# Kernel optimization log

Hardware: AMD Instinct MI355X
Metric: run time of the kernel (lower is better)

Reference implementation:

```python
import jax, jax.numpy as jnp
import numpy as np

T, H, E, I, SI, TOP_K = 4096, 2048, 16, 1024, 4096, 1


def setup_inputs() -> dict:
    key = jax.random.key(0)
    ks = jax.random.split(key, 8)
    s_h = 1.0 / np.sqrt(H)
    s_i = 1.0 / np.sqrt(I)
    s_si = 1.0 / np.sqrt(SI)
    return {
        "hidden_states": jax.random.normal(ks[0], (T, H), jnp.float32),
        "router_w": jax.random.normal(ks[1], (E, H), jnp.float32) * s_h,
        "w_gate": jax.random.normal(ks[2], (E, H, I), jnp.float32) * s_h,
        "w_up": jax.random.normal(ks[3], (E, H, I), jnp.float32) * s_h,
        "w_down": jax.random.normal(ks[4], (E, I, H), jnp.float32) * s_i,
        "ws_gate": jax.random.normal(ks[5], (H, SI), jnp.float32) * s_h,
        "ws_up": jax.random.normal(ks[6], (H, SI), jnp.float32) * s_h,
        "ws_down": jax.random.normal(ks[7], (SI, H), jnp.float32) * s_si,
    }


def reference(hidden_states, router_w, w_gate, w_up, w_down, ws_gate, ws_up, ws_down):
    x = hidden_states  # [T, H]
    # Router: logits -> top-k -> sigmoid weights (Llama4RenormalizeMoeRoutingMethod)
    logits = jnp.einsum("th,eh->te", x, router_w)              # [T, E]
    top_vals, top_idx = jax.lax.top_k(logits, TOP_K)            # [T, K]
    weights = jax.nn.sigmoid(top_vals)                          # [T, K]
    # dispatch[t, e] = router weight if expert e selected for token t, else 0
    onehot = jax.nn.one_hot(top_idx, E, dtype=x.dtype)          # [T, K, E]
    dispatch = jnp.einsum("tke,tk->te", onehot, weights)        # [T, E]
    # Routed experts: router weight applied on input (commutes through the
    # linear gate/up projections as a per-(t,e) scalar applied before SiLU).
    g = jnp.einsum("th,ehi->tei", x, w_gate) * dispatch[:, :, None]  # [T, E, I]
    u = jnp.einsum("th,ehi->tei", x, w_up) * dispatch[:, :, None]    # [T, E, I]
    act = jax.nn.silu(g) * u                                          # [T, E, I]
    # Unselected experts contribute exactly 0 (act==0 there), so summing over
    # E in the down projection is the combine step.
    routed = jnp.einsum("tei,eih->th", act, w_down)             # [T, H]
    # Shared expert (SiLU-gated MLP on the unscaled hidden states)
    shared = (jax.nn.silu(x @ ws_gate) * (x @ ws_up)) @ ws_down  # [T, H]
    return shared + routed
```

## Files before the change

kernel.cpp:

```cpp
#include <hip/hip_runtime.h>
#include <hip/hip_bf16.h>

typedef unsigned short u16;
typedef unsigned int   u32;
typedef __attribute__((ext_vector_type(8))) short short8;
typedef __attribute__((ext_vector_type(4))) float f32x4;

#define T_TOK 4096
#define HDIM  2048
#define NEXP  16
#define IDIM  1024
#define SIDIM 4096
#define RCAP  6144
#define NTIL  48

#define O_WT      0u
#define O_EIDX    16384u
#define O_CNT     32768u
#define O_POS     32832u
#define O_PADOFF  32896u
#define O_TILEEXP 33024u
#define O_TOKROW  33280u
#define O_XBF     65536u
#define O_XSC     (O_XBF  + 2u*T_TOK*HDIM)
#define O_ACTS    (O_XSC  + 2u*RCAP*HDIM)
#define O_ACTR    (O_ACTS + 2u*T_TOK*SIDIM)
#define O_WSGT    (O_ACTR + 2u*RCAP*IDIM)
#define O_WSUT    (O_WSGT + 2u*SIDIM*HDIM)
#define O_WSDT    (O_WSUT + 2u*SIDIM*HDIM)

__device__ __forceinline__ u16 f2b(float f) {
  u32 u = __float_as_uint(f);
  u = (u + 0x7FFFu + ((u >> 16) & 1u)) >> 16;
  return (u16)u;
}

#define GLDS16(g, l) __builtin_amdgcn_global_load_lds( \
    (const __attribute__((address_space(1))) void*)(g), \
    (__attribute__((address_space(3))) void*)(l), 16, 0, 0)
#define BARX() __builtin_amdgcn_s_barrier()
#define SETPRIO(x) __builtin_amdgcn_s_setprio(x)
#define WAITVM(n) asm volatile("s_waitcnt vmcnt(" #n ")" ::: "memory")

__global__ __launch_bounds__(256) void router_k(
    const float* __restrict__ x, const float* __restrict__ rw,
    float* __restrict__ wt, int* __restrict__ eidx, int* __restrict__ cnt,
    u16* __restrict__ xbf) {
  int w = threadIdx.x >> 6, l = threadIdx.x & 63;
  int t = blockIdx.x * 4 + w;
  double acc[NEXP];
#pragma unroll
  for (int e = 0; e < NEXP; ++e) acc[e] = 0.0;
  const float* xp = x + (size_t)t * HDIM;
  u16* xo = xbf + (size_t)t * HDIM;
  for (int hb = 0; hb < HDIM; hb += 256) {
    float4 xv = *(const float4*)(xp + hb + l * 4);
    uint2 o;
    o.x = (u32)f2b(xv.x) | ((u32)f2b(xv.y) << 16);
    o.y = (u32)f2b(xv.z) | ((u32)f2b(xv.w) << 16);
    *(uint2*)(xo + hb + l * 4) = o;
#pragma unroll
    for (int e = 0; e < NEXP; ++e) {
      float4 wv = *(const float4*)(rw + (size_t)e * HDIM + hb + l * 4);
      acc[e] += (double)xv.x * wv.x + (double)xv.y * wv.y
              + (double)xv.z * wv.z + (double)xv.w * wv.w;
    }
  }
#pragma unroll
  for (int e = 0; e < NEXP; ++e) {
    double v = acc[e];
#pragma unroll
    for (int off = 32; off; off >>= 1) v += __shfl_xor(v, off, 64);
    acc[e] = v;
  }
  if (l == 0) {
    double best = acc[0]; int be = 0;
#pragma unroll
    for (int e = 1; e < NEXP; ++e) if (acc[e] > best) { best = acc[e]; be = e; }
    wt[t] = 1.0f / (1.0f + __expf(-(float)best));
    eidx[t] = be;
    atomicAdd(&cnt[be], 1);
  }
}

__global__ void scan_k(const int* __restrict__ cnt, int* __restrict__ pad_off,
                       int* __restrict__ tile_exp, int* __restrict__ pos,
                       int* __restrict__ tok_row) {
  if (threadIdx.x == 0) {
    for (int i = 0; i < 64; ++i) tile_exp[i] = -1;
    int run = 0;
    for (int e = 0; e < NEXP; ++e) {
      pad_off[e] = run;
      int pc = ((cnt[e] + 127) >> 7) << 7;
      for (int tt = run >> 7; tt < (run + pc) >> 7; ++tt) tile_exp[tt] = e;
      run += pc;
      pos[e] = 0;
    }
    pad_off[NEXP] = run;
  }
  for (int i = threadIdx.x; i < RCAP; i += 256) tok_row[i] = -1;
}

__global__ void assign_k(const int* __restrict__ eidx, const int* __restrict__ pad_off,
                         int* __restrict__ pos, int* __restrict__ tok_row) {
  int t = blockIdx.x * 256 + threadIdx.x;
  if (t >= T_TOK) return;
  int e = eidx[t];
  int r = atomicAdd(&pos[e], 1);
  tok_row[pad_off[e] + r] = t;
}

__global__ __launch_bounds__(256) void gather_k(
    const float* __restrict__ x, const float* __restrict__ wt,
    const int* __restrict__ tok_row, u16* __restrict__ xsc) {
  int g = blockIdx.x;
  int tid = threadIdx.x;
  u16* dst = xsc + (size_t)g * HDIM;
  int t = tok_row[g];
  if (t < 0) {
    uint2 z; z.x = 0u; z.y = 0u;
#pragma unroll
    for (int i = 0; i < 2; ++i) *(uint2*)(dst + i * 1024 + tid * 4) = z;
  } else {
    float s = wt[t];
    const float* src = x + (size_t)t * HDIM;
#pragma unroll
    for (int i = 0; i < 2; ++i) {
      int c = i * 1024 + tid * 4;
      float4 v = *(const float4*)(src + c);
      uint2 o;
      o.x = (u32)f2b(v.x * s) | ((u32)f2b(v.y * s) << 16);
      o.y = (u32)f2b(v.z * s) | ((u32)f2b(v.w * s) << 16);
      *(uint2*)(dst + c) = o;
    }
  }
}

__device__ __forceinline__ void conv_tile(
    const float* __restrict__ src, u16* __restrict__ dst, int K, int N,
    int bx, int ky, u32 (*lt)[36], int tid) {
  const int n0 = bx * 64, k0 = ky * 64;
  const int l = tid & 63, w = tid >> 6;
  const float* sp = src + (size_t)(k0 + w * 16) * N + n0 + l;
  u32 p[8];
#pragma unroll
  for (int i = 0; i < 8; ++i) {
    float a = sp[(size_t)(2 * i) * N];
    float b = sp[(size_t)(2 * i + 1) * N];
    p[i] = (u32)f2b(a) | ((u32)f2b(b) << 16);
  }
  *(uint4*)&lt[l][w * 8 + 0] = make_uint4(p[0], p[1], p[2], p[3]);
  *(uint4*)&lt[l][w * 8 + 4] = make_uint4(p[4], p[5], p[6], p[7]);
  __syncthreads();
  const int c = tid & 7, n2 = tid >> 3;
#pragma unroll
  for (int rnd = 0; rnd < 2; ++rnd) {
    int n = n2 + rnd * 32;
    uint4 v = *(const uint4*)&lt[n][c * 4];
    *(uint4*)(dst + (size_t)(n0 + n) * K + k0 + c * 8) = v;
  }
}

__global__ __launch_bounds__(256) void megaconv(
    const float* __restrict__ wsg, const float* __restrict__ wsu,
    const float* __restrict__ wsd, u16* wsgT, u16* wsuT, u16* wsdT) {
  __shared__ u32 lt[64][36];
  int idx = blockIdx.x, tid = threadIdx.x;
  if (idx < 2048) {
    conv_tile(wsg, wsgT, 2048, 4096, idx & 63, idx >> 6, lt, tid);
  } else if (idx < 4096) { idx -= 2048;
    conv_tile(wsu, wsuT, 2048, 4096, idx & 63, idx >> 6, lt, tid);
  } else { idx -= 4096;
    conv_tile(wsd, wsdT, 4096, 2048, idx & 31, idx >> 5, lt, tid);
  }
}


__global__ __launch_bounds__(512, 2) void gu_sh8(
    const u16* __restrict__ A, const u16* __restrict__ Bg, const u16* __restrict__ Bu,
    u16* __restrict__ act) {
  extern __shared__ u16 sm[];
  u16* As  = sm;
  u16* Bsm = sm + 32768;
  const int bid = blockIdx.x;
  const int xcd = bid & 7, bi = bid >> 3;
  const int bx = xcd * 4 + (bi & 3), by = bi >> 2;
  const int m0 = by * 256, c0 = bx * 128;
  const int tid = threadIdx.x, l = tid & 63, wid = tid >> 6;
  const int wm = wid >> 1, wn = wid & 1;

  const int cpos = tid & 3, rr = tid >> 2;
  const int gc = (cpos ^ ((rr >> 1) & 3)) * 8;
  const u16* aS0 = A + (size_t)(m0 + rr) * HDIM + gc;
  const u16* aS1 = A + (size_t)(m0 + 128 + rr) * HDIM + gc;
  const int mat = (rr >> 6) & 1;
  const u16* bbase = mat ? Bu : Bg;
  const u16* bS0 = bbase + (size_t)(c0 + (rr & 63)) * HDIM + gc;
  const u16* bS1 = bbase + (size_t)(c0 + 64 + (rr & 63)) * HDIM + gc;
  const int ld0 = tid * 8, ld1 = (512 + tid) * 8;

#define STA_G(bb, kh, koff) do { \
    GLDS16(aS0 + (koff) + (kh) * 32, As + ((bb) * 2 + (kh)) * 8192 + ld0); \
    GLDS16(aS1 + (koff) + (kh) * 32, As + ((bb) * 2 + (kh)) * 8192 + ld1); } while (0)
#define STB_G(bb, kh, koff) do { \
    GLDS16(bS0 + (koff) + (kh) * 32, Bsm + ((bb) * 2 + (kh)) * 8192 + ld0); \
    GLDS16(bS1 + (koff) + (kh) * 32, Bsm + ((bb) * 2 + (kh)) * 8192 + ld1); } while (0)

  const int fch = ((l >> 4) ^ ((l >> 1) & 3)) * 8;
  int aoff[4], boff[8];
#pragma unroll
  for (int mf = 0; mf < 4; ++mf) aoff[mf] = (wm * 64 + mf * 16 + (l & 15)) * 32 + fch;
#pragma unroll
  for (int i = 0; i < 8; ++i) {
    int v = wn * 128 + (i >> 2) * 64 + (i & 3) * 16 + (l & 15);
    boff[i] = v * 32 + fch;
  }
#define LDA_G(bb, kh) do { const u16* s_ = As + ((bb) * 2 + (kh)) * 8192; \
    af[0] = *(const short8*)(s_ + aoff[0]); af[1] = *(const short8*)(s_ + aoff[1]); \
    af[2] = *(const short8*)(s_ + aoff[2]); af[3] = *(const short8*)(s_ + aoff[3]); } while (0)
#define LDB_G(bb, kh, h, d) do { const u16* s_ = Bsm + ((bb) * 2 + (kh)) * 8192; \
    d[0] = *(const short8*)(s_ + boff[(h) * 4 + 0]); d[1] = *(const short8*)(s_ + boff[(h) * 4 + 1]); \
    d[2] = *(const short8*)(s_ + boff[(h) * 4 + 2]); d[3] = *(const short8*)(s_ + boff[(h) * 4 + 3]); } while (0)
#define MM32_G() do { SETPRIO(1); \
    _Pragma("unroll") for (int mf = 0; mf < 4; ++mf) { \
      _Pragma("unroll") for (int nf = 0; nf < 4; ++nf) \
        acc[mf][nf] = __builtin_amdgcn_mfma_f32_16x16x32_bf16(af[mf], bfrA[nf], acc[mf][nf], 0, 0, 0); \
      _Pragma("unroll") for (int nf = 0; nf < 4; ++nf) \
        acc[mf][4 + nf] = __builtin_amdgcn_mfma_f32_16x16x32_bf16(af[mf], bfrB[nf], acc[mf][4 + nf], 0, 0, 0); \
    } SETPRIO(0); } while (0)

  f32x4 acc[4][8];
#pragma unroll
  for (int i = 0; i < 4; ++i)
#pragma unroll
    for (int j = 0; j < 8; ++j)
#pragma unroll
      for (int r = 0; r < 4; ++r) acc[i][j][r] = 0.0f;
  short8 af[4], bfrA[4], bfrB[4];

  STA_G(0, 0, 0); STB_G(0, 0, 0); STA_G(0, 1, 0); STB_G(0, 1, 0);
  WAITVM(4); BARX();
  const int NT = HDIM / 64;
  for (int t = 0; t < NT - 1; ++t) {
    const int b = t & 1, nb = b ^ 1, kn = (t + 1) * 64;
    LDA_G(b, 0); LDB_G(b, 0, 0, bfrA); LDB_G(b, 0, 1, bfrB);
    STA_G(nb, 0, kn); STB_G(nb, 0, kn);
    MM32_G(); WAITVM(4); BARX();
    LDA_G(b, 1); LDB_G(b, 1, 0, bfrA); LDB_G(b, 1, 1, bfrB);
    STA_G(nb, 1, kn); STB_G(nb, 1, kn);
    MM32_G(); WAITVM(4); BARX();
  }
  { const int b = (NT - 1) & 1;
    LDA_G(b, 0); LDB_G(b, 0, 0, bfrA); LDB_G(b, 0, 1, bfrB);
    MM32_G(); WAITVM(0); BARX();
    LDA_G(b, 1); LDB_G(b, 1, 0, bfrA); LDB_G(b, 1, 1, bfrB);
    MM32_G();
  }
#pragma unroll
  for (int mf = 0; mf < 4; ++mf)
#pragma unroll
    for (int nf = 0; nf < 4; ++nf) {
      int col = c0 + wn * 64 + nf * 16 + (l & 15);
      int rowb = m0 + wm * 64 + mf * 16 + (l >> 4) * 4;
#pragma unroll
      for (int r = 0; r < 4; ++r) {
        float g = acc[mf][nf][r], u = acc[mf][4 + nf][r];
        float s = g / (1.0f + __expf(-g));
        act[(size_t)(rowb + r) * SIDIM + col] = f2b(s * u);
      }
    }
#undef STA_G
#undef STB_G
#undef LDA_G
#undef LDB_G
#undef MM32_G
}

__global__ __launch_bounds__(512, 2) void dn_sh8(
    const u16* __restrict__ A, const u16* __restrict__ B, float* __restrict__ out) {
  extern __shared__ u16 sm[];
  u16* As  = sm;
  u16* Bsm = sm + 32768;
  const int bid = blockIdx.x;
  const int xcd = bid & 7, bi = bid >> 3;
  const int bx = xcd * 2 + (bi & 1), by = bi >> 1;
  const int m0 = by * 256, c0 = bx * 128;
  const int tid = threadIdx.x, l = tid & 63, wid = tid >> 6;
  const int wm = wid >> 1, wn = wid & 1;

  const int cpos = tid & 3, rr = tid >> 2;
  const int gc = (cpos ^ ((rr >> 1) & 3)) * 8;
  const u16* aS0 = A + (size_t)(m0 + rr) * SIDIM + gc;
  const u16* aS1 = A + (size_t)(m0 + 128 + rr) * SIDIM + gc;
  const u16* bS  = B + (size_t)(c0 + rr) * SIDIM + gc;
  const int ld0 = tid * 8, ld1 = (512 + tid) * 8;

#define STA_D(bb, kh, koff) do { \
    GLDS16(aS0 + (koff) + (kh) * 32, As + ((bb) * 2 + (kh)) * 8192 + ld0); \
    GLDS16(aS1 + (koff) + (kh) * 32, As + ((bb) * 2 + (kh)) * 8192 + ld1); } while (0)
#define STB_D(bb, kh, koff) \
    GLDS16(bS + (koff) + (kh) * 32, Bsm + ((bb) * 2 + (kh)) * 4096 + ld0)

  const int fch = ((l >> 4) ^ ((l >> 1) & 3)) * 8;
  int aoff[4], boff[4];
#pragma unroll
  for (int mf = 0; mf < 4; ++mf) aoff[mf] = (wm * 64 + mf * 16 + (l & 15)) * 32 + fch;
#pragma unroll
  for (int i = 0; i < 4; ++i) {
    int v = wn * 64 + (i >> 1) * 32 + (i & 1) * 16 + (l & 15);
    boff[i] = v * 32 + fch;
  }
#define LDA_D(bb, kh) do { const u16* s_ = As + ((bb) * 2 + (kh)) * 8192; \
    af[0] = *(const short8*)(s_ + aoff[0]); af[1] = *(const short8*)(s_ + aoff[1]); \
    af[2] = *(const short8*)(s_ + aoff[2]); af[3] = *(const short8*)(s_ + aoff[3]); } while (0)
#define LDB_D(bb, kh, h, d) do { const u16* s_ = Bsm + ((bb) * 2 + (kh)) * 4096; \
    d[0] = *(const short8*)(s_ + boff[(h) * 2 + 0]); \
    d[1] = *(const short8*)(s_ + boff[(h) * 2 + 1]); } while (0)
#define MM16_D() do { SETPRIO(1); \
    _Pragma("unroll") for (int mf = 0; mf < 4; ++mf) { \
      acc[mf][0] = __builtin_amdgcn_mfma_f32_16x16x32_bf16(af[mf], bfrA[0], acc[mf][0], 0, 0, 0); \
      acc[mf][1] = __builtin_amdgcn_mfma_f32_16x16x32_bf16(af[mf], bfrA[1], acc[mf][1], 0, 0, 0); \
      acc[mf][2] = __builtin_amdgcn_mfma_f32_16x16x32_bf16(af[mf], bfrB[0], acc[mf][2], 0, 0, 0); \
      acc[mf][3] = __builtin_amdgcn_mfma_f32_16x16x32_bf16(af[mf], bfrB[1], acc[mf][3], 0, 0, 0); \
    } SETPRIO(0); } while (0)

  f32x4 acc[4][4];
#pragma unroll
  for (int i = 0; i < 4; ++i)
#pragma unroll
    for (int j = 0; j < 4; ++j)
#pragma unroll
      for (int r = 0; r < 4; ++r) acc[i][j][r] = 0.0f;
  short8 af[4], bfrA[2], bfrB[2];

  STA_D(0, 0, 0); STB_D(0, 0, 0); STA_D(0, 1, 0); STB_D(0, 1, 0);
  WAITVM(3); BARX();
  const int NT = SIDIM / 64;
  for (int t = 0; t < NT - 1; ++t) {
    const int b = t & 1, nb = b ^ 1, kn = (t + 1) * 64;
    LDA_D(b, 0); LDB_D(b, 0, 0, bfrA); LDB_D(b, 0, 1, bfrB);
    STA_D(nb, 0, kn); STB_D(nb, 0, kn);
    MM16_D(); WAITVM(3); BARX();
    LDA_D(b, 1); LDB_D(b, 1, 0, bfrA); LDB_D(b, 1, 1, bfrB);
    STA_D(nb, 1, kn); STB_D(nb, 1, kn);
    MM16_D(); WAITVM(3); BARX();
  }
  { const int b = (NT - 1) & 1;
    LDA_D(b, 0); LDB_D(b, 0, 0, bfrA); LDB_D(b, 0, 1, bfrB);
    MM16_D(); WAITVM(0); BARX();
    LDA_D(b, 1); LDB_D(b, 1, 0, bfrA); LDB_D(b, 1, 1, bfrB);
    MM16_D();
  }
#pragma unroll
  for (int mf = 0; mf < 4; ++mf)
#pragma unroll
    for (int nf = 0; nf < 4; ++nf) {
      int col = c0 + wn * 64 + (nf >> 1) * 32 + (nf & 1) * 16 + (l & 15);
      int rowb = m0 + wm * 64 + mf * 16 + (l >> 4) * 4;
#pragma unroll
      for (int r = 0; r < 4; ++r)
        out[(size_t)(rowb + r) * HDIM + col] = acc[mf][nf][r];
    }
#undef STA_D
#undef STB_D
#undef LDA_D
#undef LDB_D
#undef MM16_D
}


__global__ __launch_bounds__(256) void gu_rf(
    const u16* __restrict__ A, const float* __restrict__ Bg0, const float* __restrict__ Bu0,
    u16* __restrict__ act, const int* __restrict__ tile_exp) {
  __shared__ __align__(16) u16 As[128 * 64];
  __shared__ __align__(16) u16 Bgs[32 * 72];
  __shared__ __align__(16) u16 Bus[32 * 72];
  const int tid = threadIdx.x;
  const int l = tid & 63, w = tid >> 6;
  const int wm = w >> 1, wn = w & 1;
  const int m0 = blockIdx.y * 128, n0 = blockIdx.x * 32;
  int e = tile_exp[blockIdx.y];
  if (e < 0) return;
  size_t eo = (size_t)e * HDIM * IDIM;
  const int bcol = l & 31;
  const int krow0 = w * 16 + (l >> 5) * 8;
  const float* Bgp = Bg0 + eo + (size_t)krow0 * IDIM + n0 + bcol;
  const float* Bup = Bu0 + eo + (size_t)krow0 * IDIM + n0 + bcol;
  f32x4 accg[4], accu[4];
#pragma unroll
  for (int i = 0; i < 4; ++i)
#pragma unroll
    for (int r = 0; r < 4; ++r) { accg[i][r] = 0.0f; accu[i][r] = 0.0f; }
  const u16* Ab = A + (size_t)m0 * HDIM;

  for (int k0 = 0; k0 < HDIM; k0 += 64) {
    __syncthreads();
#pragma unroll
    for (int j = 0; j < 4; ++j) {
      int c = j * 256 + tid, r = c >> 3, cc = c & 7;
      GLDS16(Ab + (size_t)r * HDIM + k0 + ((cc ^ (r & 7)) * 8), &As[c * 8]);
    }
    {
      float g8[8], u8[8];
#pragma unroll
      for (int i = 0; i < 8; ++i) {
        g8[i] = Bgp[(size_t)(k0 + i) * IDIM];
        u8[i] = Bup[(size_t)(k0 + i) * IDIM];
      }
      uint4 pg, pu;
      pg.x = (u32)f2b(g8[0]) | ((u32)f2b(g8[1]) << 16);
      pg.y = (u32)f2b(g8[2]) | ((u32)f2b(g8[3]) << 16);
      pg.z = (u32)f2b(g8[4]) | ((u32)f2b(g8[5]) << 16);
      pg.w = (u32)f2b(g8[6]) | ((u32)f2b(g8[7]) << 16);
      *(uint4*)&Bgs[bcol * 72 + krow0] = pg;
      pu.x = (u32)f2b(u8[0]) | ((u32)f2b(u8[1]) << 16);
      pu.y = (u32)f2b(u8[2]) | ((u32)f2b(u8[3]) << 16);
      pu.z = (u32)f2b(u8[4]) | ((u32)f2b(u8[5]) << 16);
      pu.w = (u32)f2b(u8[6]) | ((u32)f2b(u8[7]) << 16);
      *(uint4*)&Bus[bcol * 72 + krow0] = pu;
    }
    __syncthreads();
#pragma unroll
    for (int kh = 0; kh < 2; ++kh) {
      const int q = kh * 4 + (l >> 4);
      short8 af[4];
#pragma unroll
      for (int mf = 0; mf < 4; ++mf) {
        int r = wm * 64 + mf * 16 + (l & 15);
        af[mf] = *(const short8*)&As[r * 64 + ((q ^ (r & 7)) * 8)];
      }
      const int n = wn * 16 + (l & 15);
      short8 bgf = *(const short8*)&Bgs[n * 72 + q * 8];
      short8 buf2 = *(const short8*)&Bus[n * 72 + q * 8];
#pragma unroll
      for (int mf = 0; mf < 4; ++mf) {
        accg[mf] = __builtin_amdgcn_mfma_f32_16x16x32_bf16(af[mf], bgf,  accg[mf], 0, 0, 0);
        accu[mf] = __builtin_amdgcn_mfma_f32_16x16x32_bf16(af[mf], buf2, accu[mf], 0, 0, 0);
      }
    }
  }
#pragma unroll
  for (int mf = 0; mf < 4; ++mf) {
    int col = n0 + wn * 16 + (l & 15);
#pragma unroll
    for (int r = 0; r < 4; ++r) {
      int row = m0 + wm * 64 + mf * 16 + (l >> 4) * 4 + r;
      float g = accg[mf][r], u = accu[mf][r];
      float s = g / (1.0f + __expf(-g));
      act[(size_t)row * IDIM + col] = f2b(s * u);
    }
  }
}

__global__ __launch_bounds__(256) void dn_rf(
    const u16* __restrict__ A, const float* __restrict__ B0, float* __restrict__ out,
    const int* __restrict__ tile_exp, const int* __restrict__ tok_row) {
  __shared__ __align__(16) u16 As[128 * 64];
  __shared__ __align__(16) u16 Bs[64 * 72];
  const int tid = threadIdx.x;
  const int l = tid & 63, w = tid >> 6;
  const int wm = w >> 1, wn = w & 1;
  const int m0 = blockIdx.y * 128, n0 = blockIdx.x * 64;
  int e = tile_exp[blockIdx.y];
  if (e < 0) return;
  const float* B = B0 + (size_t)e * IDIM * HDIM;
  f32x4 acc[4][2];
#pragma unroll
  for (int i = 0; i < 4; ++i)
#pragma unroll
    for (int j = 0; j < 2; ++j)
#pragma unroll
      for (int r = 0; r < 4; ++r) acc[i][j][r] = 0.0f;
  const u16* Ab = A + (size_t)m0 * IDIM;

  for (int k0 = 0; k0 < IDIM; k0 += 64) {
    __syncthreads();
#pragma unroll
    for (int j = 0; j < 4; ++j) {
      int c = j * 256 + tid, r = c >> 3, cc = c & 7;
      GLDS16(Ab + (size_t)r * IDIM + k0 + ((cc ^ (r & 7)) * 8), &As[c * 8]);
    }
    {
      const float* bp = B + (size_t)(k0 + w * 16) * HDIM + n0 + l;
      u16 h[16];
#pragma unroll
      for (int i = 0; i < 16; ++i) h[i] = f2b(bp[(size_t)i * HDIM]);
#pragma unroll
      for (int j = 0; j < 4; ++j) {
        uint2 v; v.x = (u32)h[4*j] | ((u32)h[4*j+1] << 16);
        v.y = (u32)h[4*j+2] | ((u32)h[4*j+3] << 16);
        *(uint2*)&Bs[l * 72 + w * 16 + j * 4] = v;
      }
    }
    __syncthreads();
#pragma unroll
    for (int kh = 0; kh < 2; ++kh) {
      const int q = kh * 4 + (l >> 4);
      short8 af[4];
#pragma unroll
      for (int mf = 0; mf < 4; ++mf) {
        int r = wm * 64 + mf * 16 + (l & 15);
        af[mf] = *(const short8*)&As[r * 64 + ((q ^ (r & 7)) * 8)];
      }
      short8 bf[2];
#pragma unroll
      for (int nf = 0; nf < 2; ++nf) {
        int n = wn * 32 + nf * 16 + (l & 15);
        bf[nf] = *(const short8*)&Bs[n * 72 + q * 8];
      }
#pragma unroll
      for (int mf = 0; mf < 4; ++mf)
#pragma unroll
        for (int nf = 0; nf < 2; ++nf)
          acc[mf][nf] = __builtin_amdgcn_mfma_f32_16x16x32_bf16(af[mf], bf[nf], acc[mf][nf], 0, 0, 0);
    }
  }
#pragma unroll
  for (int mf = 0; mf < 4; ++mf)
#pragma unroll
    for (int nf = 0; nf < 2; ++nf) {
      int col = n0 + wn * 32 + nf * 16 + (l & 15);
#pragma unroll
      for (int r = 0; r < 4; ++r) {
        int grow = m0 + wm * 64 + mf * 16 + (l >> 4) * 4 + r;
        int t = tok_row[grow];
        if (t >= 0) out[(size_t)t * HDIM + col] += acc[mf][nf][r];
      }
    }
}

extern "C" void kernel_launch(void* const* d_in, const int* in_sizes, int n_in,
                              void* d_out, int out_size, void* d_ws, size_t ws_size,
                              hipStream_t stream) {
  const float* x   = (const float*)d_in[0];
  const float* rw  = (const float*)d_in[1];
  const float* wg  = (const float*)d_in[2];
  const float* wu  = (const float*)d_in[3];
  const float* wd  = (const float*)d_in[4];
  const float* wsg = (const float*)d_in[5];
  const float* wsu = (const float*)d_in[6];
  const float* wsd = (const float*)d_in[7];
  float* out = (float*)d_out;
  char* ws = (char*)d_ws;

  float* wt     = (float*)(ws + O_WT);
  int* eidx     = (int*)(ws + O_EIDX);
  int* cnt      = (int*)(ws + O_CNT);
  int* pos      = (int*)(ws + O_POS);
  int* pad_off  = (int*)(ws + O_PADOFF);
  int* tile_exp = (int*)(ws + O_TILEEXP);
  int* tok_row  = (int*)(ws + O_TOKROW);
  u16* xbf      = (u16*)(ws + O_XBF);
  u16* xsc      = (u16*)(ws + O_XSC);
  u16* acts     = (u16*)(ws + O_ACTS);
  u16* actr     = (u16*)(ws + O_ACTR);
  u16* wsgT     = (u16*)(ws + O_WSGT);
  u16* wsuT     = (u16*)(ws + O_WSUT);
  u16* wsdT     = (u16*)(ws + O_WSDT);

  hipFuncSetAttribute((const void*)gu_sh8, hipFuncAttributeMaxDynamicSharedMemorySize, 131072);
  hipFuncSetAttribute((const void*)dn_sh8, hipFuncAttributeMaxDynamicSharedMemorySize, 98304);

  hipMemsetAsync(ws + O_CNT, 0, 128, stream);
  megaconv<<<6144, 256, 0, stream>>>(wsg, wsu, wsd, wsgT, wsuT, wsdT);
  router_k<<<T_TOK / 4, 256, 0, stream>>>(x, rw, wt, eidx, cnt, xbf);
  scan_k<<<1, 256, 0, stream>>>(cnt, pad_off, tile_exp, pos, tok_row);
  assign_k<<<T_TOK / 256, 256, 0, stream>>>(eidx, pad_off, pos, tok_row);
  gather_k<<<RCAP, 256, 0, stream>>>(x, wt, tok_row, xsc);

  gu_sh8<<<512, 512, 131072, stream>>>(xbf, wsgT, wsuT, acts);
  gu_rf<<<dim3(IDIM / 32, NTIL), 256, 0, stream>>>(xsc, wg, wu, actr, tile_exp);
  dn_sh8<<<256, 512, 98304, stream>>>(acts, wsdT, out);
  dn_rf<<<dim3(HDIM / 64, NTIL), 256, 0, stream>>>(actr, wd, out, tile_exp, tok_row);
}
```

Baseline: 572.7 us.

## Double-buffer routed expert GEMMs with direct fp32 weight LDS loads

Restructures gu_rf and dn_rf into a double-buffered pipeline. A and the fp32 expert weights are loaded asynchronously into LDS through global_load_lds, so the next k-slice is fetched while the current one feeds MFMA. Weights are now converted to bf16 at fragment-read time with v_cvt_pk_bf16_f32 instead of the per-thread scalar loads plus a software round-and-pack before the LDS store. This also adds s_setprio around the MFMA bursts and 64KB of dynamic LDS per block, which may lower occupancy.

Measured after the change: 605.8 us. +5.8%, slower.

```diff
diff --git a/kernel.cpp b/kernel.cpp
--- a/kernel.cpp
+++ b/kernel.cpp
@@ -35,6 +35,12 @@
   return (u16)u;
 }
 
+__device__ __forceinline__ u32 cvtpk(float a, float b) {
+  u32 r;
+  asm("v_cvt_pk_bf16_f32 %0, %1, %2" : "=v"(r) : "v"(a), "v"(b));
+  return r;
+}
+
 #define GLDS16(g, l) __builtin_amdgcn_global_load_lds( \
     (const __attribute__((address_space(1))) void*)(g), \
     (__attribute__((address_space(3))) void*)(l), 16, 0, 0)
@@ -372,72 +378,89 @@
 __global__ __launch_bounds__(256) void gu_rf(
     const u16* __restrict__ A, const float* __restrict__ Bg0, const float* __restrict__ Bu0,
     u16* __restrict__ act, const int* __restrict__ tile_exp) {
-  __shared__ __align__(16) u16 As[128 * 64];
-  __shared__ __align__(16) u16 Bgs[32 * 72];
-  __shared__ __align__(16) u16 Bus[32 * 72];
+  extern __shared__ __align__(16) char smraw[];
+  u16*   smA  = (u16*)smraw;
+  float* smBg = (float*)(smraw + 32768);
+  float* smBu = (float*)(smraw + 49152);
   const int tid = threadIdx.x;
-  const int l = tid & 63, w = tid >> 6;
-  const int wm = w >> 1, wn = w & 1;
+  const int l = tid & 63, w4 = tid >> 6;
+  const int wm = w4 >> 1, wn = w4 & 1;
   const int m0 = blockIdx.y * 128, n0 = blockIdx.x * 32;
   int e = tile_exp[blockIdx.y];
   if (e < 0) return;
   size_t eo = (size_t)e * HDIM * IDIM;
-  const int bcol = l & 31;
-  const int krow0 = w * 16 + (l >> 5) * 8;
-  const float* Bgp = Bg0 + eo + (size_t)krow0 * IDIM + n0 + bcol;
-  const float* Bup = Bu0 + eo + (size_t)krow0 * IDIM + n0 + bcol;
+  const float* Bg = Bg0 + eo;
+  const float* Bu = Bu0 + eo;
+  const u16* Ab = A + (size_t)m0 * HDIM;
+
+  const int bk = tid >> 3;
+  const int bn = ((tid & 7) * 4) ^ (((bk >> 3) & 1) << 4);
+
+#define STA_R(bb, kh, k0v) do { \
+    _Pragma("unroll") for (int li = 0; li < 2; ++li) { \
+      int c_ = li * 256 + tid, r_ = c_ >> 2, cp_ = c_ & 3; \
+      int gc_ = (cp_ ^ ((r_ >> 1) & 3)) * 8; \
+      GLDS16(Ab + (size_t)r_ * HDIM + (k0v) + (kh) * 32 + gc_, \
+             smA + ((bb) * 2 + (kh)) * 4096 + c_ * 8); } } while (0)
+#define STB_R(bb, kh, k0v) do { \
+    GLDS16(Bg + (size_t)((k0v) + (kh) * 32 + bk) * IDIM + n0 + bn, \
+           smBg + ((bb) * 2 + (kh)) * 1024 + tid * 4); \
+    GLDS16(Bu + (size_t)((k0v) + (kh) * 32 + bk) * IDIM + n0 + bn, \
+           smBu + ((bb) * 2 + (kh)) * 1024 + tid * 4); } while (0)
+
+  const int fch = ((l >> 4) ^ ((l >> 1) & 3)) * 8;
+  int aoff[4];
+#pragma unroll
+  for (int mf = 0; mf < 4; ++mf) aoff[mf] = (wm * 64 + mf * 16 + (l & 15)) * 32 + fch;
+  const int bnr = (wn * 16 + (l & 15)) ^ (((l >> 4) & 1) << 4);
+  const int bkb = (l >> 4) * 8;
+
   f32x4 accg[4], accu[4];
 #pragma unroll
   for (int i = 0; i < 4; ++i)
 #pragma unroll
     for (int r = 0; r < 4; ++r) { accg[i][r] = 0.0f; accu[i][r] = 0.0f; }
-  const u16* Ab = A + (size_t)m0 * HDIM;
-
-  for (int k0 = 0; k0 < HDIM; k0 += 64) {
-    __syncthreads();
-#pragma unroll
-    for (int j = 0; j < 4; ++j) {
-      int c = j * 256 + tid, r = c >> 3, cc = c & 7;
-      GLDS16(Ab + (size_t)r * HDIM + k0 + ((cc ^ (r & 7)) * 8), &As[c * 8]);
-    }
-    {
-      float g8[8], u8[8];
-#pragma unroll
-      for (int i = 0; i < 8; ++i) {
-        g8[i] = Bgp[(size_t)(k0 + i) * IDIM];
-        u8[i] = Bup[(size_t)(k0 + i) * IDIM];
-      }
-      uint4 pg, pu;
-      pg.x = (u32)f2b(g8[0]) | ((u32)f2b(g8[1]) << 16);
-      pg.y = (u32)f2b(g8[2]) | ((u32)f2b(g8[3]) << 16);
-      pg.z = (u32)f2b(g8[4]) | ((u32)f2b(g8[5]) << 16);
-      pg.w = (u32)f2b(g8[6]) | ((u32)f2b(g8[7]) << 16);
-      *(uint4*)&Bgs[bcol * 72 + krow0] = pg;
-      pu.x = (u32)f2b(u8[0]) | ((u32)f2b(u8[1]) << 16);
-      pu.y = (u32)f2b(u8[2]) | ((u32)f2b(u8[3]) << 16);
-      pu.z = (u32)f2b(u8[4]) | ((u32)f2b(u8[5]) << 16);
-      pu.w = (u32)f2b(u8[6]) | ((u32)f2b(u8[7]) << 16);
-      *(uint4*)&Bus[bcol * 72 + krow0] = pu;
-    }
-    __syncthreads();
-#pragma unroll
-    for (int kh = 0; kh < 2; ++kh) {
-      const int q = kh * 4 + (l >> 4);
-      short8 af[4];
-#pragma unroll
-      for (int mf = 0; mf < 4; ++mf) {
-        int r = wm * 64 + mf * 16 + (l & 15);
-        af[mf] = *(const short8*)&As[r * 64 + ((q ^ (r & 7)) * 8)];
-      }
-      const int n = wn * 16 + (l & 15);
-      short8 bgf = *(const short8*)&Bgs[n * 72 + q * 8];
-      short8 buf2 = *(const short8*)&Bus[n * 72 + q * 8];
-#pragma unroll
-      for (int mf = 0; mf < 4; ++mf) {
-        accg[mf] = __builtin_amdgcn_mfma_f32_16x16x32_bf16(af[mf], bgf,  accg[mf], 0, 0, 0);
-        accu[mf] = __builtin_amdgcn_mfma_f32_16x16x32_bf16(af[mf], buf2, accu[mf], 0, 0, 0);
-      }
-    }
+  short8 af[4], bgf, buf2;
+
+#define PH_READ_R(bb, kh) do { \
+    const u16* As_ = smA + ((bb) * 2 + (kh)) * 4096; \
+    af[0] = *(const short8*)(As_ + aoff[0]); af[1] = *(const short8*)(As_ + aoff[1]); \
+    af[2] = *(const short8*)(As_ + aoff[2]); af[3] = *(const short8*)(As_ + aoff[3]); \
+    const float* Bg_ = smBg + ((bb) * 2 + (kh)) * 1024; \
+    const float* Bu_ = smBu + ((bb) * 2 + (kh)) * 1024; \
+    int4 wg_, wu_; \
+    wg_.x = cvtpk(Bg_[(bkb + 0) * 32 + bnr], Bg_[(bkb + 1) * 32 + bnr]); \
+    wg_.y = cvtpk(Bg_[(bkb + 2) * 32 + bnr], Bg_[(bkb + 3) * 32 + bnr]); \
+    wg_.z = cvtpk(Bg_[(bkb + 4) * 32 + bnr], Bg_[(bkb + 5) * 32 + bnr]); \
+    wg_.w = cvtpk(Bg_[(bkb + 6) * 32 + bnr], Bg_[(bkb + 7) * 32 + bnr]); \
+    wu_.x = cvtpk(Bu_[(bkb + 0) * 32 + bnr], Bu_[(bkb + 1) * 32 + bnr]); \
+    wu_.y = cvtpk(Bu_[(bkb + 2) * 32 + bnr], Bu_[(bkb + 3) * 32 + bnr]); \
+    wu_.z = cvtpk(Bu_[(bkb + 4) * 32 + bnr], Bu_[(bkb + 5) * 32 + bnr]); \
+    wu_.w = cvtpk(Bu_[(bkb + 6) * 32 + bnr], Bu_[(bkb + 7) * 32 + bnr]); \
+    bgf  = *(short8*)&wg_; buf2 = *(short8*)&wu_; } while (0)
+#define MM_R() do { SETPRIO(1); \
+    _Pragma("unroll") for (int mf = 0; mf < 4; ++mf) { \
+      accg[mf] = __builtin_amdgcn_mfma_f32_16x16x32_bf16(af[mf], bgf,  accg[mf], 0, 0, 0); \
+      accu[mf] = __builtin_amdgcn_mfma_f32_16x16x32_bf16(af[mf], buf2, accu[mf], 0, 0, 0); \
+    } SETPRIO(0); } while (0)
+
+  STA_R(0, 0, 0); STB_R(0, 0, 0); STA_R(0, 1, 0); STB_R(0, 1, 0);
+  WAITVM(0); BARX();
+  const int NT = HDIM / 64;
+  for (int t = 0; t < NT - 1; ++t) {
+    const int b = t & 1, nb = b ^ 1, kn = (t + 1) * 64;
+    PH_READ_R(b, 0);
+    STA_R(nb, 0, kn); STB_R(nb, 0, kn);
+    MM_R(); WAITVM(4); BARX();
+    PH_READ_R(b, 1);
+    STA_R(nb, 1, kn); STB_R(nb, 1, kn);
+    MM_R(); WAITVM(4); BARX();
+  }
+  { const int b = (NT - 1) & 1;
+    PH_READ_R(b, 0);
+    MM_R(); WAITVM(0); BARX();
+    PH_READ_R(b, 1);
+    MM_R();
   }
 #pragma unroll
   for (int mf = 0; mf < 4; ++mf) {
@@ -450,20 +473,50 @@
       act[(size_t)row * IDIM + col] = f2b(s * u);
     }
   }
+#undef STA_R
+#undef STB_R
+#undef PH_READ_R
+#undef MM_R
 }
 
 __global__ __launch_bounds__(256) void dn_rf(
     const u16* __restrict__ A, const float* __restrict__ B0, float* __restrict__ out,
     const int* __restrict__ tile_exp, const int* __restrict__ tok_row) {
-  __shared__ __align__(16) u16 As[128 * 64];
-  __shared__ __align__(16) u16 Bs[64 * 72];
+  extern __shared__ __align__(16) char smraw[];
+  u16*   smA = (u16*)smraw;
+  float* smB = (float*)(smraw + 32768);
   const int tid = threadIdx.x;
-  const int l = tid & 63, w = tid >> 6;
-  const int wm = w >> 1, wn = w & 1;
+  const int l = tid & 63, w4 = tid >> 6;
+  const int wm = w4 >> 1, wn = w4 & 1;
   const int m0 = blockIdx.y * 128, n0 = blockIdx.x * 64;
   int e = tile_exp[blockIdx.y];
   if (e < 0) return;
   const float* B = B0 + (size_t)e * IDIM * HDIM;
+  const u16* Ab = A + (size_t)m0 * IDIM;
+
+#define STA_E(bb, kh, k0v) do { \
+    _Pragma("unroll") for (int li = 0; li < 2; ++li) { \
+      int c_ = li * 256 + tid, r_ = c_ >> 2, cp_ = c_ & 3; \
+      int gc_ = (cp_ ^ ((r_ >> 1) & 3)) * 8; \
+      GLDS16(Ab + (size_t)r_ * IDIM + (k0v) + (kh) * 32 + gc_, \
+             smA + ((bb) * 2 + (kh)) * 4096 + c_ * 8); } } while (0)
+#define STB_E(bb, kh, k0v) do { \
+    _Pragma("unroll") for (int li = 0; li < 2; ++li) { \
+      int s_ = li * 256 + tid, k_ = s_ >> 4; \
+      int n_ = ((s_ & 15) * 4) ^ (((k_ >> 3) & 1) << 4); \
+      GLDS16(B + (size_t)((k0v) + (kh) * 32 + k_) * HDIM + n0 + n_, \
+             smB + ((bb) * 2 + (kh)) * 2048 + s_ * 4); } } while (0)
+
+  const int fch = ((l >> 4) ^ ((l >> 1) & 3)) * 8;
+  int aoff[4];
+#pragma unroll
+  for (int mf = 0; mf < 4; ++mf) aoff[mf] = (wm * 64 + mf * 16 + (l & 15)) * 32 + fch;
+  int bnr[2];
+#pragma unroll
+  for (int nf = 0; nf < 2; ++nf)
+    bnr[nf] = (wn * 32 + nf * 16 + (l & 15)) ^ (((l >> 4) & 1) << 4);
+  const int bkb = (l >> 4) * 8;
+
   f32x4 acc[4][2];
 #pragma unroll
   for (int i = 0; i < 4; ++i)
@@ -471,49 +524,43 @@
     for (int j = 0; j < 2; ++j)
 #pragma unroll
       for (int r = 0; r < 4; ++r) acc[i][j][r] = 0.0f;
-  const u16* Ab = A + (size_t)m0 * IDIM;
-
-  for (int k0 = 0; k0 < IDIM; k0 += 64) {
-    __syncthreads();
-#pragma unroll
-    for (int j = 0; j < 4; ++j) {
-      int c = j * 256 + tid, r = c >> 3, cc = c & 7;
-      GLDS16(Ab + (size_t)r * IDIM + k0 + ((cc ^ (r & 7)) * 8), &As[c * 8]);
-    }
-    {
-      const float* bp = B + (size_t)(k0 + w * 16) * HDIM + n0 + l;
-      u16 h[16];
-#pragma unroll
-      for (int i = 0; i < 16; ++i) h[i] = f2b(bp[(size_t)i * HDIM]);
-#pragma unroll
-      for (int j = 0; j < 4; ++j) {
-        uint2 v; v.x = (u32)h[4*j] | ((u32)h[4*j+1] << 16);
-        v.y = (u32)h[4*j+2] | ((u32)h[4*j+3] << 16);
-        *(uint2*)&Bs[l * 72 + w * 16 + j * 4] = v;
-      }
-    }
-    __syncthreads();
-#pragma unroll
-    for (int kh = 0; kh < 2; ++kh) {
-      const int q = kh * 4 + (l >> 4);
-      short8 af[4];
-#pragma unroll
-      for (int mf = 0; mf < 4; ++mf) {
-        int r = wm * 64 + mf * 16 + (l & 15);
-        af[mf] = *(const short8*)&As[r * 64 + ((q ^ (r & 7)) * 8)];
-      }
-      short8 bf[2];
-#pragma unroll
-      for (int nf = 0; nf < 2; ++nf) {
-        int n = wn * 32 + nf * 16 + (l & 15);
-        bf[nf] = *(const short8*)&Bs[n * 72 + q * 8];
-      }
-#pragma unroll
-      for (int mf = 0; mf < 4; ++mf)
-#pragma unroll
-        for (int nf = 0; nf < 2; ++nf)
-          acc[mf][nf] = __builtin_amdgcn_mfma_f32_16x16x32_bf16(af[mf], bf[nf], acc[mf][nf], 0, 0, 0);
-    }
+  short8 af[4], bf[2];
+
+#define PH_READ_E(bb, kh) do { \
+    const u16* As_ = smA + ((bb) * 2 + (kh)) * 4096; \
+    af[0] = *(const short8*)(As_ + aoff[0]); af[1] = *(const short8*)(As_ + aoff[1]); \
+    af[2] = *(const short8*)(As_ + aoff[2]); af[3] = *(const short8*)(As_ + aoff[3]); \
+    const float* B_ = smB + ((bb) * 2 + (kh)) * 2048; \
+    _Pragma("unroll") for (int nf = 0; nf < 2; ++nf) { \
+      int4 w_; \
+      w_.x = cvtpk(B_[(bkb + 0) * 64 + bnr[nf]], B_[(bkb + 1) * 64 + bnr[nf]]); \
+      w_.y = cvtpk(B_[(bkb + 2) * 64 + bnr[nf]], B_[(bkb + 3) * 64 + bnr[nf]]); \
+      w_.z = cvtpk(B_[(bkb + 4) * 64 + bnr[nf]], B_[(bkb + 5) * 64 + bnr[nf]]); \
+      w_.w = cvtpk(B_[(bkb + 6) * 64 + bnr[nf]], B_[(bkb + 7) * 64 + bnr[nf]]); \
+      bf[nf] = *(short8*)&w_; } } while (0)
+#define MM_E() do { SETPRIO(1); \
+    _Pragma("unroll") for (int mf = 0; mf < 4; ++mf) { \
+      acc[mf][0] = __builtin_amdgcn_mfma_f32_16x16x32_bf16(af[mf], bf[0], acc[mf][0], 0, 0, 0); \
+      acc[mf][1] = __builtin_amdgcn_mfma_f32_16x16x32_bf16(af[mf], bf[1], acc[mf][1], 0, 0, 0); \
+    } SETPRIO(0); } while (0)
+
+  STA_E(0, 0, 0); STB_E(0, 0, 0); STA_E(0, 1, 0); STB_E(0, 1, 0);
+  WAITVM(0); BARX();
+  const int NT = IDIM / 64;
+  for (int t = 0; t < NT - 1; ++t) {
+    const int b = t & 1, nb = b ^ 1, kn = (t + 1) * 64;
+    PH_READ_E(b, 0);
+    STA_E(nb, 0, kn); STB_E(nb, 0, kn);
+    MM_E(); WAITVM(4); BARX();
+    PH_READ_E(b, 1);
+    STA_E(nb, 1, kn); STB_E(nb, 1, kn);
+    MM_E(); WAITVM(4); BARX();
+  }
+  { const int b = (NT - 1) & 1;
+    PH_READ_E(b, 0);
+    MM_E(); WAITVM(0); BARX();
+    PH_READ_E(b, 1);
+    MM_E();
   }
 #pragma unroll
   for (int mf = 0; mf < 4; ++mf)
@@ -527,6 +574,10 @@
         if (t >= 0) out[(size_t)t * HDIM + col] += acc[mf][nf][r];
       }
     }
+#undef STA_E
+#undef STB_E
+#undef PH_READ_E
+#undef MM_E
 }
 
 extern "C" void kernel_launch(void* const* d_in, const int* in_sizes, int n_in,
@@ -560,6 +611,8 @@
 
   hipFuncSetAttribute((const void*)gu_sh8, hipFuncAttributeMaxDynamicSharedMemorySize, 131072);
   hipFuncSetAttribute((const void*)dn_sh8, hipFuncAttributeMaxDynamicSharedMemorySize, 98304);
+  hipFuncSetAttribute((const void*)gu_rf, hipFuncAttributeMaxDynamicSharedMemorySize, 65536);
+  hipFuncSetAttribute((const void*)dn_rf, hipFuncAttributeMaxDynamicSharedMemorySize, 65536);
 
   hipMemsetAsync(ws + O_CNT, 0, 128, stream);
   megaconv<<<6144, 256, 0, stream>>>(wsg, wsu, wsd, wsgT, wsuT, wsdT);
@@ -569,7 +622,7 @@
   gather_k<<<RCAP, 256, 0, stream>>>(x, wt, tok_row, xsc);
 
   gu_sh8<<<512, 512, 131072, stream>>>(xbf, wsgT, wsuT, acts);
-  gu_rf<<<dim3(IDIM / 32, NTIL), 256, 0, stream>>>(xsc, wg, wu, actr, tile_exp);
+  gu_rf<<<dim3(IDIM / 32, NTIL), 256, 65536, stream>>>(xsc, wg, wu, actr, tile_exp);
   dn_sh8<<<256, 512, 98304, stream>>>(acts, wsdT, out);
-  dn_rf<<<dim3(HDIM / 64, NTIL), 256, 0, stream>>>(actr, wd, out, tile_exp, tok_row);
-}
+  dn_rf<<<dim3(HDIM / 64, NTIL), 256, 65536, stream>>>(actr, wd, out, tile_exp, tok_row);
+}
```

## Drop LDS staging in routed expert GEMMs, load fragments directly into registers

Applied to the files above, without the earlier changes.

The routed gate/up and down kernels no longer stage A and B tiles through shared memory with barriers. Each lane now loads its MFMA fragments straight from global memory and converts fp32 weights with the packed bf16 convert instruction. This removes the LDS writes, LDS reads and both barriers per k-step. In exchange, waves that share a tile each re-read it from global/L2, which raises redundant global traffic and gives up the swizzled coalesced A loads.

Result: slower. 1.017 ms (+77.5%).

```diff
diff --git a/kernel.cpp b/kernel.cpp
--- a/kernel.cpp
+++ b/kernel.cpp
@@ -35,6 +35,12 @@
   return (u16)u;
 }
 
+__device__ __forceinline__ u32 cvtpk(float a, float b) {
+  u32 r;
+  asm("v_cvt_pk_bf16_f32 %0, %1, %2" : "=v"(r) : "v"(a), "v"(b));
+  return r;
+}
+
 #define GLDS16(g, l) __builtin_amdgcn_global_load_lds( \
     (const __attribute__((address_space(1))) void*)(g), \
     (__attribute__((address_space(3))) void*)(l), 16, 0, 0)
@@ -372,9 +378,6 @@
 __global__ __launch_bounds__(256) void gu_rf(
     const u16* __restrict__ A, const float* __restrict__ Bg0, const float* __restrict__ Bu0,
     u16* __restrict__ act, const int* __restrict__ tile_exp) {
-  __shared__ __align__(16) u16 As[128 * 64];
-  __shared__ __align__(16) u16 Bgs[32 * 72];
-  __shared__ __align__(16) u16 Bus[32 * 72];
   const int tid = threadIdx.x;
   const int l = tid & 63, w = tid >> 6;
   const int wm = w >> 1, wn = w & 1;
@@ -382,72 +385,57 @@
   int e = tile_exp[blockIdx.y];
   if (e < 0) return;
   size_t eo = (size_t)e * HDIM * IDIM;
-  const int bcol = l & 31;
-  const int krow0 = w * 16 + (l >> 5) * 8;
-  const float* Bgp = Bg0 + eo + (size_t)krow0 * IDIM + n0 + bcol;
-  const float* Bup = Bu0 + eo + (size_t)krow0 * IDIM + n0 + bcol;
+  const int col = wn * 16 + (l & 15);
+  const int q0 = l >> 4;
+  const float* Bg = Bg0 + eo + n0 + col;
+  const float* Bu = Bu0 + eo + n0 + col;
+  const u16* Ar = A + (size_t)(m0 + wm * 64 + (l & 15)) * HDIM;
+
   f32x4 accg[4], accu[4];
 #pragma unroll
   for (int i = 0; i < 4; ++i)
 #pragma unroll
     for (int r = 0; r < 4; ++r) { accg[i][r] = 0.0f; accu[i][r] = 0.0f; }
-  const u16* Ab = A + (size_t)m0 * HDIM;
 
   for (int k0 = 0; k0 < HDIM; k0 += 64) {
-    __syncthreads();
-#pragma unroll
-    for (int j = 0; j < 4; ++j) {
-      int c = j * 256 + tid, r = c >> 3, cc = c & 7;
-      GLDS16(Ab + (size_t)r * HDIM + k0 + ((cc ^ (r & 7)) * 8), &As[c * 8]);
-    }
-    {
-      float g8[8], u8[8];
-#pragma unroll
-      for (int i = 0; i < 8; ++i) {
-        g8[i] = Bgp[(size_t)(k0 + i) * IDIM];
-        u8[i] = Bup[(size_t)(k0 + i) * IDIM];
+    short8 af[2][4];
+    float bg[2][8], bu[2][8];
+#pragma unroll
+    for (int kh = 0; kh < 2; ++kh) {
+      const int kq = k0 + (kh * 4 + q0) * 8;
+#pragma unroll
+      for (int mf = 0; mf < 4; ++mf)
+        af[kh][mf] = *(const short8*)(Ar + (size_t)(mf * 16) * HDIM + kq);
+#pragma unroll
+      for (int j = 0; j < 8; ++j) {
+        bg[kh][j] = Bg[(size_t)(kq + j) * IDIM];
+        bu[kh][j] = Bu[(size_t)(kq + j) * IDIM];
       }
-      uint4 pg, pu;
-      pg.x = (u32)f2b(g8[0]) | ((u32)f2b(g8[1]) << 16);
-      pg.y = (u32)f2b(g8[2]) | ((u32)f2b(g8[3]) << 16);
-      pg.z = (u32)f2b(g8[4]) | ((u32)f2b(g8[5]) << 16);
-      pg.w = (u32)f2b(g8[6]) | ((u32)f2b(g8[7]) << 16);
-      *(uint4*)&Bgs[bcol * 72 + krow0] = pg;
-      pu.x = (u32)f2b(u8[0]) | ((u32)f2b(u8[1]) << 16);
-      pu.y = (u32)f2b(u8[2]) | ((u32)f2b(u8[3]) << 16);
-      pu.z = (u32)f2b(u8[4]) | ((u32)f2b(u8[5]) << 16);
-      pu.w = (u32)f2b(u8[6]) | ((u32)f2b(u8[7]) << 16);
-      *(uint4*)&Bus[bcol * 72 + krow0] = pu;
-    }
-    __syncthreads();
+    }
 #pragma unroll
     for (int kh = 0; kh < 2; ++kh) {
-      const int q = kh * 4 + (l >> 4);
-      short8 af[4];
+      int4 pg, pu;
+      pg.x = cvtpk(bg[kh][0], bg[kh][1]); pg.y = cvtpk(bg[kh][2], bg[kh][3]);
+      pg.z = cvtpk(bg[kh][4], bg[kh][5]); pg.w = cvtpk(bg[kh][6], bg[kh][7]);
+      pu.x = cvtpk(bu[kh][0], bu[kh][1]); pu.y = cvtpk(bu[kh][2], bu[kh][3]);
+      pu.z = cvtpk(bu[kh][4], bu[kh][5]); pu.w = cvtpk(bu[kh][6], bu[kh][7]);
+      short8 bgf = *(short8*)&pg, buf2 = *(short8*)&pu;
 #pragma unroll
       for (int mf = 0; mf < 4; ++mf) {
-        int r = wm * 64 + mf * 16 + (l & 15);
-        af[mf] = *(const short8*)&As[r * 64 + ((q ^ (r & 7)) * 8)];
+        accg[mf] = __builtin_amdgcn_mfma_f32_16x16x32_bf16(af[kh][mf], bgf,  accg[mf], 0, 0, 0);
+        accu[mf] = __builtin_amdgcn_mfma_f32_16x16x32_bf16(af[kh][mf], buf2, accu[mf], 0, 0, 0);
       }
-      const int n = wn * 16 + (l & 15);
-      short8 bgf = *(const short8*)&Bgs[n * 72 + q * 8];
-      short8 buf2 = *(const short8*)&Bus[n * 72 + q * 8];
-#pragma unroll
-      for (int mf = 0; mf < 4; ++mf) {
-        accg[mf] = __builtin_amdgcn_mfma_f32_16x16x32_bf16(af[mf], bgf,  accg[mf], 0, 0, 0);
-        accu[mf] = __builtin_amdgcn_mfma_f32_16x16x32_bf16(af[mf], buf2, accu[mf], 0, 0, 0);
-      }
     }
   }
 #pragma unroll
   for (int mf = 0; mf < 4; ++mf) {
-    int col = n0 + wn * 16 + (l & 15);
+    int ocol = n0 + wn * 16 + (l & 15);
 #pragma unroll
     for (int r = 0; r < 4; ++r) {
       int row = m0 + wm * 64 + mf * 16 + (l >> 4) * 4 + r;
       float g = accg[mf][r], u = accu[mf][r];
       float s = g / (1.0f + __expf(-g));
-      act[(size_t)row * IDIM + col] = f2b(s * u);
+      act[(size_t)row * IDIM + ocol] = f2b(s * u);
     }
   }
 }
@@ -455,15 +443,19 @@
 __global__ __launch_bounds__(256) void dn_rf(
     const u16* __restrict__ A, const float* __restrict__ B0, float* __restrict__ out,
     const int* __restrict__ tile_exp, const int* __restrict__ tok_row) {
-  __shared__ __align__(16) u16 As[128 * 64];
-  __shared__ __align__(16) u16 Bs[64 * 72];
   const int tid = threadIdx.x;
   const int l = tid & 63, w = tid >> 6;
   const int wm = w >> 1, wn = w & 1;
   const int m0 = blockIdx.y * 128, n0 = blockIdx.x * 64;
   int e = tile_exp[blockIdx.y];
   if (e < 0) return;
-  const float* B = B0 + (size_t)e * IDIM * HDIM;
+  const float* B = B0 + (size_t)e * IDIM * HDIM + n0;
+  const int q0 = l >> 4;
+  const u16* Ar = A + (size_t)(m0 + wm * 64 + (l & 15)) * IDIM;
+  int bcol[2];
+#pragma unroll
+  for (int nf = 0; nf < 2; ++nf) bcol[nf] = wn * 32 + nf * 16 + (l & 15);
+
   f32x4 acc[4][2];
 #pragma unroll
   for (int i = 0; i < 4; ++i)
@@ -471,48 +463,37 @@
     for (int j = 0; j < 2; ++j)
 #pragma unroll
       for (int r = 0; r < 4; ++r) acc[i][j][r] = 0.0f;
-  const u16* Ab = A + (size_t)m0 * IDIM;
 
   for (int k0 = 0; k0 < IDIM; k0 += 64) {
-    __syncthreads();
-#pragma unroll
-    for (int j = 0; j < 4; ++j) {
-      int c = j * 256 + tid, r = c >> 3, cc = c & 7;
-      GLDS16(Ab + (size_t)r * IDIM + k0 + ((cc ^ (r & 7)) * 8), &As[c * 8]);
-    }
-    {
-      const float* bp = B + (size_t)(k0 + w * 16) * HDIM + n0 + l;
-      u16 h[16];
-#pragma unroll
-      for (int i = 0; i < 16; ++i) h[i] = f2b(bp[(size_t)i * HDIM]);
-#pragma unroll
-      for (int j = 0; j < 4; ++j) {
-        uint2 v; v.x = (u32)h[4*j] | ((u32)h[4*j+1] << 16);
-        v.y = (u32)h[4*j+2] | ((u32)h[4*j+3] << 16);
-        *(uint2*)&Bs[l * 72 + w * 16 + j * 4] = v;
+    short8 af[2][4];
+    float bb[2][2][8];
+#pragma unroll
+    for (int kh = 0; kh < 2; ++kh) {
+      const int kq = k0 + (kh * 4 + q0) * 8;
+#pragma unroll
+      for (int mf = 0; mf < 4; ++mf)
+        af[kh][mf] = *(const short8*)(Ar + (size_t)(mf * 16) * IDIM + kq);
+#pragma unroll
+      for (int nf = 0; nf < 2; ++nf)
+#pragma unroll
+        for (int j = 0; j < 8; ++j)
+          bb[kh][nf][j] = B[(size_t)(kq + j) * HDIM + bcol[nf]];
+    }
+#pragma unroll
+    for (int kh = 0; kh < 2; ++kh) {
+      short8 bf[2];
+#pragma unroll
+      for (int nf = 0; nf < 2; ++nf) {
+        int4 p;
+        p.x = cvtpk(bb[kh][nf][0], bb[kh][nf][1]); p.y = cvtpk(bb[kh][nf][2], bb[kh][nf][3]);
+        p.z = cvtpk(bb[kh][nf][4], bb[kh][nf][5]); p.w = cvtpk(bb[kh][nf][6], bb[kh][nf][7]);
+        bf[nf] = *(short8*)&p;
       }
-    }
-    __syncthreads();
-#pragma unroll
-    for (int kh = 0; kh < 2; ++kh) {
-      const int q = kh * 4 + (l >> 4);
-      short8 af[4];
-#pragma unroll
-      for (int mf = 0; mf < 4; ++mf) {
-        int r = wm * 64 + mf * 16 + (l & 15);
-        af[mf] = *(const short8*)&As[r * 64 + ((q ^ (r & 7)) * 8)];
-      }
-      short8 bf[2];
-#pragma unroll
-      for (int nf = 0; nf < 2; ++nf) {
-        int n = wn * 32 + nf * 16 + (l & 15);
-        bf[nf] = *(const short8*)&Bs[n * 72 + q * 8];
-      }
 #pragma unroll
       for (int mf = 0; mf < 4; ++mf)
 #pragma unroll
         for (int nf = 0; nf < 2; ++nf)
-          acc[mf][nf] = __builtin_amdgcn_mfma_f32_16x16x32_bf16(af[mf], bf[nf], acc[mf][nf], 0, 0, 0);
+          acc[mf][nf] = __builtin_amdgcn_mfma_f32_16x16x32_bf16(af[kh][mf], bf[nf], acc[mf][nf], 0, 0, 0);
     }
   }
 #pragma unroll
```
